# Performance work log

Hardware: AMD Instinct MI355X
Metric: run time of the kernel (lower is better)

Reference implementation:

```python
import jax, jax.numpy as jnp
import numpy as np

HIDDEN = 1024
NUM_HEADS = 16
HEAD_DIM = HIDDEN // NUM_HEADS
WINDOW = 512


def setup_inputs() -> dict:
    key = jax.random.key(0)
    ks = jax.random.split(key, 6)
    b, s = 2, 4096
    x = jax.random.normal(ks[0], (b, s, HIDDEN), dtype=jnp.float32)
    attention_mask = jnp.ones((b, s), dtype=jnp.int32)
    scale = 1.0 / np.sqrt(HIDDEN)
    Wq = jax.random.normal(ks[1], (HIDDEN, HIDDEN), dtype=jnp.float32) * scale
    Wk = jax.random.normal(ks[2], (HIDDEN, HIDDEN), dtype=jnp.float32) * scale
    Wv = jax.random.normal(ks[3], (HIDDEN, HIDDEN), dtype=jnp.float32) * scale
    Wo = jax.random.normal(ks[4], (HIDDEN, HIDDEN), dtype=jnp.float32) * scale
    return {"x": x, "attention_mask": attention_mask,
            "Wq": Wq, "Wk": Wk, "Wv": Wv, "Wo": Wo}


def reference(x, attention_mask, Wq, Wk, Wv, Wo):
    b, s, d = x.shape
    # nn.Linear computes x @ W.T
    q = (x @ Wq.T).reshape(b, s, NUM_HEADS, HEAD_DIM).transpose(0, 2, 1, 3)
    k = (x @ Wk.T).reshape(b, s, NUM_HEADS, HEAD_DIM).transpose(0, 2, 1, 3)
    v = (x @ Wv.T).reshape(b, s, NUM_HEADS, HEAD_DIM).transpose(0, 2, 1, 3)
    # [b,h,s,s] scores
    scores = jnp.einsum('bhqd,bhkd->bhqk', q, k) / np.sqrt(HEAD_DIM)
    # causal sliding-window mask: allow j <= i and j >= i - window + 1
    i = jnp.arange(s)[:, None]
    j = jnp.arange(s)[None, :]
    window_mask = (j <= i) & (j >= i - WINDOW + 1)  # [s,s]
    neg_inf = jnp.finfo(scores.dtype).min
    scores = jnp.where(window_mask[None, None], scores, neg_inf)
    pad = attention_mask.astype(bool)[:, None, None, :]  # [b,1,1,s]
    scores = jnp.where(pad, scores, neg_inf)
    probs = jax.nn.softmax(scores, axis=-1)
    out = jnp.einsum('bhqk,bhkd->bhqd', probs, v)
    out = out.transpose(0, 2, 1, 3).reshape(b, s, d)
    return out @ Wo.T
```

## Files before the change

kernel.cpp:

```cpp
#include <hip/hip_runtime.h>
#include <cstdint>
#include <cstddef>

#define HID 1024
#define SEQ 4096
#define NB  2
#define NH  16
#define HD  64
#define WIN 512
#define TOK (NB*SEQ)

typedef _Float16 f16x8 __attribute__((ext_vector_type(8)));
typedef _Float16 f16x4 __attribute__((ext_vector_type(4)));
typedef float    f32x4 __attribute__((ext_vector_type(4)));

__global__ __launch_bounds__(256)
void convert_kernel(const float* __restrict__ X, const float* __restrict__ w0,
                    const float* __restrict__ w1, const float* __restrict__ w2,
                    const float* __restrict__ w3,
                    _Float16* __restrict__ Xh, _Float16* __restrict__ Wh) {
  const int bi = blockIdx.x;
  const float* src; _Float16* dst; size_t off;
  if (bi < 4096) {
    src = X; dst = Xh; off = (size_t)bi * 2048;
  } else {
    const int wi = bi - 4096, z = wi >> 9;
    src = (z == 0) ? w0 : (z == 1) ? w1 : (z == 2) ? w2 : w3;
    dst = Wh + (size_t)z * HID * HID;
    off = (size_t)(wi & 511) * 2048;
  }
  const size_t i = off + (size_t)threadIdx.x * 8;
  f32x4 a = *(const f32x4*)(src + i);
  f32x4 b = *(const f32x4*)(src + i + 4);
  f16x8 o;
#pragma unroll
  for (int r = 0; r < 4; ++r) { o[r] = (_Float16)a[r]; o[r+4] = (_Float16)b[r]; }
  *(f16x8*)(dst + i) = o;
}

__device__ __forceinline__ void gload16(const void* g, void* lds) {
  __builtin_amdgcn_global_load_lds(
      (__attribute__((address_space(1))) void*)(void*)g,
      (__attribute__((address_space(3))) void*)lds, 16, 0, 0);
}

__device__ __forceinline__ void gemm_mainloop(
    const _Float16* __restrict__ A, const _Float16* __restrict__ W,
    _Float16* sA, _Float16* sB, f32x4 (&acc)[4][4], int m0, int n0) {
  const int tid  = threadIdx.x;
  const int lane = tid & 63;
  const int wave = tid >> 6;
  const int wm = wave >> 1, wn = wave & 1;
  const int l15 = lane & 15, quad = lane >> 4;

  const int o0 = tid * 16;
  const int o1 = o0 + 4096;
  const _Float16* a0 = A + (size_t)(m0 + (o0 >> 6)) * HID + ((o0 & 63) >> 1);
  const _Float16* a1 = A + (size_t)(m0 + (o1 >> 6)) * HID + ((o1 & 63) >> 1);
  const _Float16* w0 = W + (size_t)(n0 + (o0 >> 6)) * HID + ((o0 & 63) >> 1);
  const _Float16* w1 = W + (size_t)(n0 + (o1 >> 6)) * HID + ((o1 & 63) >> 1);
  _Float16* la0 = sA + (o0 >> 1);
  _Float16* la1 = sA + (o1 >> 1);
  _Float16* lb0 = sB + (o0 >> 1);
  _Float16* lb1 = sB + (o1 >> 1);

  const int aoff = (wm*64 + l15)*32 + quad*8;
  const int boff = (wn*64 + l15)*32 + quad*8;

  for (int k0 = 0; k0 < HID; k0 += 64) {
    __syncthreads();
    gload16(a0 + k0,      la0);
    gload16(a1 + k0,      la1);
    gload16(a0 + k0 + 32, la0 + 4096);
    gload16(a1 + k0 + 32, la1 + 4096);
    gload16(w0 + k0,      lb0);
    gload16(w1 + k0,      lb1);
    gload16(w0 + k0 + 32, lb0 + 4096);
    gload16(w1 + k0 + 32, lb1 + 4096);
    __syncthreads();
#pragma unroll
    for (int s = 0; s < 2; ++s) {
      const int sb = s * 4096;
      f16x8 af[4], wf[4];
#pragma unroll
      for (int t = 0; t < 4; ++t) {
        af[t] = *(const f16x8*)(sA + sb + aoff + t*512);
        wf[t] = *(const f16x8*)(sB + sb + boff + t*512);
      }
#pragma unroll
      for (int i = 0; i < 4; ++i)
#pragma unroll
        for (int j = 0; j < 4; ++j)
          acc[i][j] = __builtin_amdgcn_mfma_f32_16x16x32_f16(af[i], wf[j], acc[i][j], 0, 0, 0);
    }
  }
}

__global__ __launch_bounds__(256, 3)
void gemm_qkv_kernel(const _Float16* __restrict__ X,
                     const _Float16* __restrict__ Wh,
                     _Float16* __restrict__ Q,
                     _Float16* __restrict__ Kb,
                     _Float16* __restrict__ Vt) {
  __shared__ __align__(16) _Float16 sA[128*64];
  __shared__ __align__(16) _Float16 sB[128*64];
  const int i  = blockIdx.x;
  const int g  = i & 7;
  const int j  = i >> 3;
  const int mi = j & 7;
  const int c  = j >> 3;
  const int z  = c >> 3;
  const int n0 = (c & 7) * 128;
  const int m0 = (g*8 + mi) * 128;
  const _Float16* W = Wh + (size_t)z * HID * HID;
  f32x4 acc[4][4] = {};
  gemm_mainloop(X, W, sA, sB, acc, m0, n0);

  const int tid  = threadIdx.x;
  const int lane = tid & 63;
  const int wave = tid >> 6;
  const int wm = wave >> 1, wn = wave & 1;
  const int l15 = lane & 15, quad = lane >> 4;

  if (z < 2) {
    _Float16* C = (z == 0) ? Q : Kb;
    const float scl = (z == 0) ? 0.18033688011f : 1.0f;
#pragma unroll
    for (int tm = 0; tm < 4; ++tm)
#pragma unroll
      for (int tn = 0; tn < 4; ++tn) {
        const int row = m0 + wm*64 + tm*16 + quad*4;
        const int col = n0 + wn*64 + tn*16 + l15;
#pragma unroll
        for (int r = 0; r < 4; ++r)
          C[(size_t)(row + r)*HID + col] = (_Float16)(acc[tm][tn][r] * scl);
      }
  } else {
#pragma unroll
    for (int tm = 0; tm < 4; ++tm)
#pragma unroll
      for (int tn = 0; tn < 4; ++tn) {
        const int row = m0 + wm*64 + tm*16 + quad*4;
        const int col = n0 + wn*64 + tn*16 + l15;
        f16x4 v;
#pragma unroll
        for (int r = 0; r < 4; ++r) v[r] = (_Float16)acc[tm][tn][r];
        *(f16x4*)(Vt + (size_t)col*TOK + row) = v;
      }
  }
}

__global__ __launch_bounds__(256, 3)
void gemm_o_kernel(const _Float16* __restrict__ A,
                   const _Float16* __restrict__ Wo,
                   float* __restrict__ C) {
  __shared__ __align__(16) _Float16 sA[128*64];
  __shared__ __align__(16) _Float16 sB[128*64];
  const int i  = blockIdx.x;
  const int g  = i & 7;
  const int j  = i >> 3;
  const int mi = j & 7;
  const int n0 = (j >> 3) * 128;
  const int m0 = (g*8 + mi) * 128;
  f32x4 acc[4][4] = {};
  gemm_mainloop(A, Wo, sA, sB, acc, m0, n0);

  const int tid  = threadIdx.x;
  const int lane = tid & 63;
  const int wave = tid >> 6;
  const int wm = wave >> 1, wn = wave & 1;
  const int l15 = lane & 15, quad = lane >> 4;
#pragma unroll
  for (int tm = 0; tm < 4; ++tm)
#pragma unroll
    for (int tn = 0; tn < 4; ++tn) {
      const int row = m0 + wm*64 + tm*16 + quad*4;
      const int col = n0 + wn*64 + tn*16 + l15;
#pragma unroll
      for (int r = 0; r < 4; ++r)
        C[(size_t)(row + r)*HID + col] = acc[tm][tn][r];
    }
}

__global__ __launch_bounds__(512, 4)
void attn_kernel(const _Float16* __restrict__ Q, const _Float16* __restrict__ Kb,
                 const _Float16* __restrict__ Vt, const int* __restrict__ AM,
                 _Float16* __restrict__ O) {
  __shared__ __align__(16) _Float16 sK[128*64];
  __shared__ __align__(16) _Float16 sV[64*128];
  __shared__ __align__(16) _Float16 sP[8*32*64];
  __shared__ int sOK;

  const int bi = blockIdx.x;
  const int g  = bi & 7;
  const int jj = bi >> 3;
  const int combo = g*4 + (jj >> 4);
  const int h = combo & 15, b = combo >> 4;
  const int qb = jj & 15;

  const int tid  = threadIdx.x;
  const int lane = tid & 63, wave = tid >> 6;
  const int l15 = lane & 15, quad = lane >> 4;

  const int q0 = qb * 256;
  const int qw = q0 + wave * 32;

  const int swz = l15 & 7;
  const int cA8 = ((quad ^ swz) << 3);
  const int cB8 = (((quad + 4) ^ swz) << 3);

  f16x8 qf[2][2];
#pragma unroll
  for (int ns = 0; ns < 2; ++ns) {
    const size_t qbse = (size_t)(b*SEQ + qw + ns*16 + l15)*HID + h*HD + quad*8;
    qf[ns][0] = *(const f16x8*)(Q + qbse);
    qf[ns][1] = *(const f16x8*)(Q + qbse + 32);
  }

  int stage_lo = (q0 - (WIN - 1));
  stage_lo = (stage_lo < 0) ? 0 : (stage_lo & ~127);
  const int nst = (q0 + 256 - stage_lo) >> 7;

  if (tid == 0) sOK = 1;
  __syncthreads();
  {
    int ok = 1;
    for (int j = stage_lo + tid; j < q0 + 256; j += 512) ok &= (AM[b*SEQ + j] != 0);
    if (!ok) sOK = 0;
  }
  __syncthreads();
  const bool allok = (sOK != 0);

  const int prow = tid >> 3;
  const int pc   = tid & 7;
  const int pco  = ((pc ^ (prow & 7)) << 3);
  f16x8 pk0, pk1, pv0, pv1;
  {
    const _Float16* kp = Kb + (size_t)(b*SEQ + stage_lo + prow)*HID + h*HD + pco;
    pk0 = *(const f16x8*)kp;
    pk1 = *(const f16x8*)(kp + (size_t)64*HID);
    const _Float16* vp = Vt + (size_t)(h*HD + prow)*TOK + b*SEQ + stage_lo + pco;
    pv0 = *(const f16x8*)vp;
    pv1 = *(const f16x8*)(vp + 64);
  }

  float l_run[2] = {0.0f, 0.0f};
  f32x4 o[4][2] = {};
  _Float16* myP = sP + wave * (32*64);

  for (int st = 0; st < nst; ++st) {
    const int j0st = stage_lo + st*128;
    __syncthreads();
    *(f16x8*)(sK + prow*64 + pc*8)        = pk0;
    *(f16x8*)(sK + (64 + prow)*64 + pc*8) = pk1;
    *(f16x8*)(sV + prow*128 + pc*8)       = pv0;
    *(f16x8*)(sV + prow*128 + 64 + pc*8)  = pv1;
    __syncthreads();
    if (st + 1 < nst) {
      const int jn = j0st + 128;
      const _Float16* kp = Kb + (size_t)(b*SEQ + jn + prow)*HID + h*HD + pco;
      pk0 = *(const f16x8*)kp;
      pk1 = *(const f16x8*)(kp + (size_t)64*HID);
      const _Float16* vp = Vt + (size_t)(h*HD + prow)*TOK + b*SEQ + jn + pco;
      pv0 = *(const f16x8*)vp;
      pv1 = *(const f16x8*)(vp + 64);
    }

#pragma unroll
    for (int s = 0; s < 2; ++s) {
      const int j0 = j0st + s*64;
      if (j0 > qw + 31 || j0 + 63 < qw - (WIN - 1)) continue;
      const bool interior = (j0 + 63 <= qw) && (j0 >= qw - (WIN - 32));

      f32x4 sc[4][2] = {};
#pragma unroll
      for (int t = 0; t < 4; ++t) {
        const f16x8 kf0 = *(const f16x8*)(sK + (s*64 + t*16 + l15)*64 + cA8);
        const f16x8 kf1 = *(const f16x8*)(sK + (s*64 + t*16 + l15)*64 + cB8);
        sc[t][0] = __builtin_amdgcn_mfma_f32_16x16x32_f16(kf0, qf[0][0], sc[t][0], 0, 0, 0);
        sc[t][0] = __builtin_amdgcn_mfma_f32_16x16x32_f16(kf1, qf[0][1], sc[t][0], 0, 0, 0);
        sc[t][1] = __builtin_amdgcn_mfma_f32_16x16x32_f16(kf0, qf[1][0], sc[t][1], 0, 0, 0);
        sc[t][1] = __builtin_amdgcn_mfma_f32_16x16x32_f16(kf1, qf[1][1], sc[t][1], 0, 0, 0);
      }

      if (!allok) {
#pragma unroll
        for (int t = 0; t < 4; ++t)
#pragma unroll
          for (int r = 0; r < 4; ++r) {
            const float ad = (AM[b*SEQ + j0 + t*16 + quad*4 + r] == 0) ? -2e30f : 0.0f;
            sc[t][0][r] += ad;
            sc[t][1][r] += ad;
          }
      }

#pragma unroll
      for (int ns = 0; ns < 2; ++ns) {
        if (!interior) {
          const int i = qw + ns*16 + l15;
#pragma unroll
          for (int t = 0; t < 4; ++t)
#pragma unroll
            for (int r = 0; r < 4; ++r) {
              const int j = j0 + t*16 + quad*4 + r;
              const bool valid = (unsigned)(i - j) < WIN;
              sc[t][ns][r] = valid ? sc[t][ns][r] : -1e30f;
            }
        }
        float sum = 0.0f;
#pragma unroll
        for (int t = 0; t < 4; ++t) {
          f16x4 pvv;
#pragma unroll
          for (int r = 0; r < 4; ++r) {
            const float p = __builtin_amdgcn_exp2f(sc[t][ns][r]);
            sum += p;
            pvv[r] = (_Float16)p;
          }
          const int paddr = (ns*16 + l15)*64 + (((2*t + (quad >> 1)) ^ swz) << 3) + (quad & 1)*4;
          *(f16x4*)(myP + paddr) = pvv;
        }
        sum += __shfl_xor(sum, 16, 64);
        sum += __shfl_xor(sum, 32, 64);
        l_run[ns] += sum;
      }

      const f16x8 pf00 = *(const f16x8*)(myP + l15*64 + cA8);
      const f16x8 pf01 = *(const f16x8*)(myP + l15*64 + cB8);
      const f16x8 pf10 = *(const f16x8*)(myP + (16 + l15)*64 + cA8);
      const f16x8 pf11 = *(const f16x8*)(myP + (16 + l15)*64 + cB8);
#pragma unroll
      for (int dt = 0; dt < 4; ++dt) {
        const f16x8 vf0 = *(const f16x8*)(sV + (dt*16 + l15)*128 + s*64 + cA8);
        const f16x8 vf1 = *(const f16x8*)(sV + (dt*16 + l15)*128 + s*64 + cB8);
        o[dt][0] = __builtin_amdgcn_mfma_f32_16x16x32_f16(vf0, pf00, o[dt][0], 0, 0, 0);
        o[dt][0] = __builtin_amdgcn_mfma_f32_16x16x32_f16(vf1, pf01, o[dt][0], 0, 0, 0);
        o[dt][1] = __builtin_amdgcn_mfma_f32_16x16x32_f16(vf0, pf10, o[dt][1], 0, 0, 0);
        o[dt][1] = __builtin_amdgcn_mfma_f32_16x16x32_f16(vf1, pf11, o[dt][1], 0, 0, 0);
      }
    }
  }

  const float inv[2] = {1.0f / fmaxf(l_run[0], 1e-30f), 1.0f / fmaxf(l_run[1], 1e-30f)};
#pragma unroll
  for (int ns = 0; ns < 2; ++ns) {
    const size_t ob = (size_t)(b*SEQ + qw + ns*16 + l15)*HID + h*HD + quad*4;
#pragma unroll
    for (int dt = 0; dt < 4; ++dt) {
      f16x4 v;
#pragma unroll
      for (int r = 0; r < 4; ++r) v[r] = (_Float16)(o[dt][ns][r] * inv[ns]);
      *(f16x4*)(O + ob + dt*16) = v;
    }
  }
}

extern "C" void kernel_launch(void* const* d_in, const int* in_sizes, int n_in,
                              void* d_out, int out_size, void* d_ws, size_t ws_size,
                              hipStream_t stream) {
  const float* X  = (const float*)d_in[0];
  const int*   AM = (const int*)d_in[1];
  const float* Wq = (const float*)d_in[2];
  const float* Wk = (const float*)d_in[3];
  const float* Wv = (const float*)d_in[4];
  const float* Wo = (const float*)d_in[5];
  float* out = (float*)d_out;

  _Float16* Xh = (_Float16*)d_ws;
  _Float16* Wh = Xh + (size_t)TOK*HID;
  _Float16* Qb = Wh + (size_t)4*HID*HID;
  _Float16* Kb = Qb + (size_t)TOK*HID;
  _Float16* Vt = Kb + (size_t)TOK*HID;
  _Float16* AO = Vt + (size_t)TOK*HID;

  convert_kernel<<<dim3(4096 + 4*512), dim3(256), 0, stream>>>(X, Wq, Wk, Wv, Wo, Xh, Wh);
  gemm_qkv_kernel<<<dim3(1536), dim3(256), 0, stream>>>(Xh, Wh, Qb, Kb, Vt);
  attn_kernel<<<dim3(512), dim3(512), 0, stream>>>(Qb, Kb, Vt, AM, AO);
  gemm_o_kernel<<<dim3(512), dim3(256), 0, stream>>>(AO, Wh + (size_t)3*HID*HID, out);
}
```

Baseline: 218.9 us.

## Replace QKV GEMM with 256x256-tile, 8-wave, multi-phase pipelined kernel

The QKV projection GEMM moves from 128x128 tiles with 4 waves to 256x256 tiles with 8 waves. Each K-step is split into eight phases that interleave global-to-LDS staging of the next sub-tiles with MFMA work, using explicit vmcnt waits, raw s_barrier, setprio and XOR-swizzled LDS layouts. The goal is to hide memory latency, cut per-tile global traffic through higher reuse, and avoid LDS bank conflicts. In exchange it uses 128KB of LDS and many registers per block, and relies on hand-tuned wait counts that are fragile.

```diff
diff --git a/kernel.cpp b/kernel.cpp
--- a/kernel.cpp
+++ b/kernel.cpp
@@ -44,6 +44,148 @@
       (__attribute__((address_space(3))) void*)lds, 16, 0, 0);
 }
 
+#define VMW_(n) asm volatile("s_waitcnt vmcnt(" #n ")" ::: "memory")
+#define VMW(n) VMW_(n)
+
+#define STG(GP, RP) {                                                         \
+    gload16((GP) + (size_t)srow*HID + scol,     (RP) + ldo0);                 \
+    gload16((GP) + (size_t)(srow+8)*HID + scol, (RP) + ldo1);                 \
+  }
+
+#define GPHASE(BF, QM, QN, VMN, STAGE) do {                                   \
+    f16x8 af[4][2], bv[2][2];                                                 \
+    const _Float16* Ah = sAb[BF][QM];                                         \
+    const _Float16* Bh = sBb[BF][QN];                                         \
+    _Pragma("unroll")                                                         \
+    for (int mm = 0; mm < 4; ++mm) {                                          \
+      const int ar = (wr*16 + mm*32 + l15) * 64;                              \
+      af[mm][0] = *(const f16x8*)(Ah + ar + ((quad ^ swl) << 3));             \
+      af[mm][1] = *(const f16x8*)(Ah + ar + (((4 + quad) ^ swl) << 3));       \
+    }                                                                         \
+    _Pragma("unroll")                                                         \
+    for (int nn = 0; nn < 2; ++nn) {                                          \
+      const int br = (nn*64 + wc*16 + l15) * 64;                              \
+      bv[nn][0] = *(const f16x8*)(Bh + br + ((quad ^ swl) << 3));             \
+      bv[nn][1] = *(const f16x8*)(Bh + br + (((4 + quad) ^ swl) << 3));       \
+    }                                                                         \
+    STAGE                                                                     \
+    __builtin_amdgcn_s_barrier();                                             \
+    __builtin_amdgcn_s_setprio(1);                                            \
+    _Pragma("unroll")                                                         \
+    for (int mm = 0; mm < 4; ++mm)                                            \
+      _Pragma("unroll")                                                       \
+      for (int nn = 0; nn < 2; ++nn) {                                        \
+        acc[QM*4+mm][QN*2+nn] = __builtin_amdgcn_mfma_f32_16x16x32_f16(       \
+            af[mm][0], bv[nn][0], acc[QM*4+mm][QN*2+nn], 0, 0, 0);            \
+        acc[QM*4+mm][QN*2+nn] = __builtin_amdgcn_mfma_f32_16x16x32_f16(       \
+            af[mm][1], bv[nn][1], acc[QM*4+mm][QN*2+nn], 0, 0, 0);            \
+      }                                                                       \
+    __builtin_amdgcn_s_setprio(0);                                            \
+    VMW(VMN);                                                                 \
+    __builtin_amdgcn_s_barrier();                                             \
+    asm volatile("" ::: "memory");                                            \
+  } while (0)
+
+__global__ __launch_bounds__(512, 2)
+void gemm_qkv8p_kernel(const _Float16* __restrict__ X,
+                       const _Float16* __restrict__ Wh,
+                       _Float16* __restrict__ Q,
+                       _Float16* __restrict__ Kb,
+                       _Float16* __restrict__ Vt) {
+  __shared__ __align__(16) _Float16 sAb[2][2][128*64];
+  __shared__ __align__(16) _Float16 sBb[2][2][128*64];
+
+  const int bid = blockIdx.x;
+  const int xcd = bid & 7, idx = bid >> 3;
+  const int mt = xcd*4 + (idx & 3);
+  const int nt = idx >> 2;
+  const int M0  = mt * 256;
+  const int N0g = nt * 256;
+  const int z   = N0g >> 10;
+  const int N0c = N0g & 1023;
+
+  const _Float16* Arow = X  + (size_t)M0 * HID;
+  const _Float16* Brow = Wh + (size_t)z * HID * HID + (size_t)N0c * HID;
+
+  const int tid  = threadIdx.x;
+  const int lane = tid & 63, wave = tid >> 6;
+  const int wr = wave >> 2, wc = wave & 3;
+  const int l15 = lane & 15, quad = lane >> 4;
+  const int swl = l15 & 7;
+
+  const int srow = wave*16 + (lane >> 3);
+  const int scol = ((lane & 7) ^ (lane >> 3)) << 3;
+  const int ldo0 = (wave*128 + lane) * 8;
+  const int ldo1 = ldo0 + 64*8;
+
+  f32x4 acc[8][4] = {};
+
+  STG(Brow,               sBb[0][0]);
+  STG(Arow,               sAb[0][0]);
+  STG(Arow + 128*HID,     sAb[0][1]);
+  STG(Brow + 128*HID,     sBb[0][1]);
+  STG(Brow + 64,          sBb[1][0]);
+  STG(Arow + 64,          sAb[1][0]);
+  VMW(8);
+  __builtin_amdgcn_s_barrier();
+  asm volatile("" ::: "memory");
+
+#pragma unroll 1
+  for (int t = 0; t < 14; t += 2) {
+    const int k1 = (t+1)*64, k2 = (t+2)*64, k3 = (t+3)*64;
+    GPHASE(0, 0, 0, 8, STG(Arow + 128*HID + k1, sAb[1][1]));
+    GPHASE(0, 1, 0, 8, STG(Brow + 128*HID + k1, sBb[1][1]));
+    GPHASE(0, 0, 1, 8, STG(Brow + k2,           sBb[0][0]));
+    GPHASE(0, 1, 1, 8, STG(Arow + k2,           sAb[0][0]));
+    GPHASE(1, 0, 0, 8, STG(Arow + 128*HID + k2, sAb[0][1]));
+    GPHASE(1, 1, 0, 8, STG(Brow + 128*HID + k2, sBb[0][1]));
+    GPHASE(1, 0, 1, 8, STG(Brow + k3,           sBb[1][0]));
+    GPHASE(1, 1, 1, 8, STG(Arow + k3,           sAb[1][0]));
+  }
+  {
+    const int k1 = 15*64;
+    GPHASE(0, 0, 0, 8, STG(Arow + 128*HID + k1, sAb[1][1]));
+    GPHASE(0, 1, 0, 8, STG(Brow + 128*HID + k1, sBb[1][1]));
+    GPHASE(0, 0, 1, 8, ;);
+    GPHASE(0, 1, 1, 4, ;);
+  }
+  {
+    GPHASE(1, 0, 0, 2, ;);
+    GPHASE(1, 1, 0, 0, ;);
+    GPHASE(1, 0, 1, 0, ;);
+    GPHASE(1, 1, 1, 0, ;);
+  }
+
+  if (z < 2) {
+    _Float16* C = (z == 0) ? Q : Kb;
+    const float scl = (z == 0) ? 0.18033688011f : 1.0f;
+#pragma unroll
+    for (int mf = 0; mf < 8; ++mf) {
+      const int row = M0 + (mf >> 2)*128 + wr*16 + (mf & 3)*32 + quad*4;
+#pragma unroll
+      for (int nf = 0; nf < 4; ++nf) {
+        const int col = N0c + (nf >> 1)*128 + (nf & 1)*64 + wc*16 + l15;
+#pragma unroll
+        for (int r = 0; r < 4; ++r)
+          C[(size_t)(row + r)*HID + col] = (_Float16)(acc[mf][nf][r] * scl);
+      }
+    }
+  } else {
+#pragma unroll
+    for (int mf = 0; mf < 8; ++mf) {
+      const int row = M0 + (mf >> 2)*128 + wr*16 + (mf & 3)*32 + quad*4;
+#pragma unroll
+      for (int nf = 0; nf < 4; ++nf) {
+        const int col = N0c + (nf >> 1)*128 + (nf & 1)*64 + wc*16 + l15;
+        f16x4 v;
+#pragma unroll
+        for (int r = 0; r < 4; ++r) v[r] = (_Float16)acc[mf][nf][r];
+        *(f16x4*)(Vt + (size_t)col*TOK + row) = v;
+      }
+    }
+  }
+}
+
 __device__ __forceinline__ void gemm_mainloop(
     const _Float16* __restrict__ A, const _Float16* __restrict__ W,
     _Float16* sA, _Float16* sB, f32x4 (&acc)[4][4], int m0, int n0) {
@@ -93,60 +235,6 @@
         for (int j = 0; j < 4; ++j)
           acc[i][j] = __builtin_amdgcn_mfma_f32_16x16x32_f16(af[i], wf[j], acc[i][j], 0, 0, 0);
     }
-  }
-}
-
-__global__ __launch_bounds__(256, 3)
-void gemm_qkv_kernel(const _Float16* __restrict__ X,
-                     const _Float16* __restrict__ Wh,
-                     _Float16* __restrict__ Q,
-                     _Float16* __restrict__ Kb,
-                     _Float16* __restrict__ Vt) {
-  __shared__ __align__(16) _Float16 sA[128*64];
-  __shared__ __align__(16) _Float16 sB[128*64];
-  const int i  = blockIdx.x;
-  const int g  = i & 7;
-  const int j  = i >> 3;
-  const int mi = j & 7;
-  const int c  = j >> 3;
-  const int z  = c >> 3;
-  const int n0 = (c & 7) * 128;
-  const int m0 = (g*8 + mi) * 128;
-  const _Float16* W = Wh + (size_t)z * HID * HID;
-  f32x4 acc[4][4] = {};
-  gemm_mainloop(X, W, sA, sB, acc, m0, n0);
-
-  const int tid  = threadIdx.x;
-  const int lane = tid & 63;
-  const int wave = tid >> 6;
-  const int wm = wave >> 1, wn = wave & 1;
-  const int l15 = lane & 15, quad = lane >> 4;
-
-  if (z < 2) {
-    _Float16* C = (z == 0) ? Q : Kb;
-    const float scl = (z == 0) ? 0.18033688011f : 1.0f;
-#pragma unroll
-    for (int tm = 0; tm < 4; ++tm)
-#pragma unroll
-      for (int tn = 0; tn < 4; ++tn) {
-        const int row = m0 + wm*64 + tm*16 + quad*4;
-        const int col = n0 + wn*64 + tn*16 + l15;
-#pragma unroll
-        for (int r = 0; r < 4; ++r)
-          C[(size_t)(row + r)*HID + col] = (_Float16)(acc[tm][tn][r] * scl);
-      }
-  } else {
-#pragma unroll
-    for (int tm = 0; tm < 4; ++tm)
-#pragma unroll
-      for (int tn = 0; tn < 4; ++tn) {
-        const int row = m0 + wm*64 + tm*16 + quad*4;
-        const int col = n0 + wn*64 + tn*16 + l15;
-        f16x4 v;
-#pragma unroll
-        for (int r = 0; r < 4; ++r) v[r] = (_Float16)acc[tm][tn][r];
-        *(f16x4*)(Vt + (size_t)col*TOK + row) = v;
-      }
   }
 }
 
@@ -374,7 +462,7 @@
   _Float16* AO = Vt + (size_t)TOK*HID;
 
   convert_kernel<<<dim3(4096 + 4*512), dim3(256), 0, stream>>>(X, Wq, Wk, Wv, Wo, Xh, Wh);
-  gemm_qkv_kernel<<<dim3(1536), dim3(256), 0, stream>>>(Xh, Wh, Qb, Kb, Vt);
+  gemm_qkv8p_kernel<<<dim3(384), dim3(512), 0, stream>>>(Xh, Wh, Qb, Kb, Vt);
   attn_kernel<<<dim3(512), dim3(512), 0, stream>>>(Qb, Kb, Vt, AM, AO);
   gemm_o_kernel<<<dim3(512), dim3(256), 0, stream>>>(AO, Wh + (size_t)3*HID*HID, out);
 }
```

Measured after the change: 244.4 us. +11.7%, slower.
